# Kernel optimization log

Hardware: AMD Instinct MI355X
Metric: run time of the kernel (lower is better)

The kernel has to match this reference:

```python
import jax, jax.numpy as jnp
import numpy as np

B, T, D = 8, 1024, 1024
SEM = D // 2          # sem_dim_size
STR = D - SEM         # str_dim_size
HALF = SEM // 2       # per-direction semantic slice


def setup_inputs() -> dict:
    key = jax.random.key(0)
    ks = jax.random.split(key, 8)
    s = lambda d: 1.0 / np.sqrt(d)
    return {
        "input": jax.random.normal(ks[0], (B, T, D), jnp.float32),
        "Wtp": jax.random.normal(ks[1], (STR, STR), jnp.float32) * s(STR),
        "btp": jnp.zeros((STR,), jnp.float32),
        "Wtc": jax.random.normal(ks[2], (STR, STR), jnp.float32) * s(STR),
        "btc": jnp.zeros((STR,), jnp.float32),
        "wfi": jax.random.normal(ks[3], (STR,), jnp.float32) * s(STR),
        "Wbil": jax.random.normal(ks[4], (STR, STR), jnp.float32) * s(STR),
        "exparam": jax.random.normal(ks[5], (1, 1, SEM), jnp.float32) * s(SEM),
        "Wfz": jax.random.normal(ks[6], (SEM, 3 * SEM), jnp.float32) * s(3 * SEM),
        "bfz": jnp.zeros((SEM,), jnp.float32),
    }


def reference(input, Wtp, btp, Wtc, btc, wfi, Wbil, exparam, Wfz, bfz):
    b, t, d = input.shape
    dt = input.dtype
    # bidirectional split: interleaved fwd/bwd halves -> semantic / structural views
    x = input.reshape(b, t, 2, d // 2)
    sem_v = jnp.concatenate([x[:, :, 0, :HALF], x[:, :, 1, :HALF]], axis=2)  # (B,T,SEM)
    str_v = jnp.concatenate([x[:, :, 0, HALF:], x[:, :, 1, HALF:]], axis=2)  # (B,T,STR)

    tp = jnp.tanh(str_v @ Wtp.T + btp)
    tc = jnp.tanh(str_v @ Wtc.T + btc)
    # bilinear matrix attention: tp W tc^T -> (B,T,T)
    f_ij = jnp.tanh(jnp.einsum('btd,de,bse->bts', tp, Wbil, tc))
    f_i = jnp.exp(jnp.tanh(str_v @ wfi))  # root scores (B,T)

    eye = jnp.eye(t, dtype=dt)
    A = jnp.exp(f_ij) * (1.0 - eye)             # zero diagonal
    col_sum = jnp.sum(A, axis=1)                # (B,T) in-degree sums
    L = -A + col_sum[:, :, None] * eye          # graph Laplacian
    L_bar = L.at[:, 0, :].set(f_i)              # replace first row with root scores
    LLinv = jnp.linalg.inv(L_bar)               # (B,T,T)

    d0 = f_i * LLinv[:, :, 0]                   # root marginals (B,T)
    diag = jnp.diagonal(LLinv, axis1=-2, axis2=-1)  # (B,T)
    tmp1 = A * diag[:, None, :]                 # A_ij * LLinv_jj
    tmp2 = A * jnp.swapaxes(LLinv, 1, 2)        # A_ij * LLinv_ji
    mask1 = jnp.concatenate([jnp.zeros((b, t, 1), dt), jnp.ones((b, t, t - 1), dt)], axis=2)
    mask2 = jnp.concatenate([jnp.zeros((b, 1, t), dt), jnp.ones((b, t - 1, t), dt)], axis=1)
    dx = mask1 * tmp1 - mask2 * tmp2            # edge marginals (B,T,T)

    d_full = jnp.concatenate([d0[:, None, :], dx], axis=1)   # (B,T+1,T)
    df = jnp.swapaxes(d_full, 1, 2)                          # (B,T,T+1)
    ssr = jnp.concatenate([jnp.broadcast_to(exparam, (b, 1, SEM)), sem_v], axis=1)
    pinp = jnp.einsum('btk,bkd->btd', df, ssr)   # parent-weighted features
    cinp = jnp.einsum('bts,bsd->btd', dx, sem_v) # child-weighted features
    finp = jnp.concatenate([sem_v, pinp, cinp], axis=2)      # (B,T,3*SEM)
    out = jax.nn.relu(finp @ Wfz.T + bfz)
    return (out, df)
```

## Files before the change

kernel.cpp:

```cpp
#include <hip/hip_runtime.h>
#include <math.h>

#define TT 1024
#define NB 64

typedef float f32x4 __attribute__((ext_vector_type(4)));
typedef __bf16 bf16x8 __attribute__((ext_vector_type(8)));

__device__ __forceinline__ float4 ld4(const float* p){ return *(const float4*)p; }
__device__ __forceinline__ float rdlane(float v, int lane){
  return __int_as_float(__builtin_amdgcn_readlane(__float_as_int(v), lane));
}
__device__ __forceinline__ unsigned short bf16rne(float x){
  unsigned u = __float_as_uint(x);
  return (unsigned short)((u + 0x7FFF + ((u >> 16) & 1)) >> 16);
}

template<int EPI, int OUTBF>
__global__ __launch_bounds__(256)
void mgemm_k(const unsigned short* __restrict__ A, const unsigned short* __restrict__ B,
             void* __restrict__ Cv, int K, int lda, int ldb, int ldc,
             long sA, long sB, long sC,
             const float* __restrict__ bias,
             const float* __restrict__ e1, long sE1, const float* __restrict__ e2)
{
  const int bz = blockIdx.z;
  A += (long)bz * sA; B += (long)bz * sB;
  __shared__ char lds[12288];
  char* As = lds;
  char* Bs = lds + 4096;
  const int tid = threadIdx.x;
  const int l = tid & 63, wid = tid >> 6;
  const int wr = wid >> 1, wc = wid & 1;
  const int m0 = blockIdx.y * 64, n0 = blockIdx.x * 128;
  const int lrow = l & 15, lslot = (l >> 4) << 4;
  f32x4 acc[2][4] = {};

  for (int kk = 0; kk < K; kk += 32) {
    {
      int row = tid >> 2, c16 = (tid & 3) << 4;
      int sw = c16 ^ (((row >> 1) & 3) << 4);
      uint4 va = *(const uint4*)(A + (long)(m0 + row) * lda + kk + (c16 >> 1));
      *(uint4*)(As + row * 64 + sw) = va;
    }
#pragma unroll
    for (int i = 0; i < 2; ++i) {
      int idx = i * 256 + tid;
      int row = idx >> 2, c16 = (idx & 3) << 4;
      int sw = c16 ^ (((row >> 1) & 3) << 4);
      uint4 vb = *(const uint4*)(B + (long)(n0 + row) * ldb + kk + (c16 >> 1));
      *(uint4*)(Bs + row * 64 + sw) = vb;
    }
    __syncthreads();
    bf16x8 af[2], bfr[4];
#pragma unroll
    for (int t = 0; t < 2; ++t) {
      int ra = wr * 32 + t * 16 + lrow;
      af[t]  = *(const bf16x8*)(As + ra * 64 + (lslot ^ (((ra >> 1) & 3) << 4)));
    }
#pragma unroll
    for (int t = 0; t < 4; ++t) {
      int rb = wc * 64 + t * 16 + lrow;
      bfr[t] = *(const bf16x8*)(Bs + rb * 64 + (lslot ^ (((rb >> 1) & 3) << 4)));
    }
#pragma unroll
    for (int mi = 0; mi < 2; ++mi)
#pragma unroll
      for (int ni = 0; ni < 4; ++ni)
        acc[mi][ni] = __builtin_amdgcn_mfma_f32_16x16x32_bf16(af[mi], bfr[ni], acc[mi][ni], 0, 0, 0);
    __syncthreads();
  }

  float* Cf = (float*)Cv; unsigned short* Cb = (unsigned short*)Cv;
  if (OUTBF) Cb += (long)bz * sC; else Cf += (long)bz * sC;
  if (e1) e1 += (long)bz * sE1;
#pragma unroll
  for (int mi = 0; mi < 2; ++mi)
#pragma unroll
  for (int ni = 0; ni < 4; ++ni)
#pragma unroll
  for (int r = 0; r < 4; ++r) {
    int m = m0 + wr * 32 + mi * 16 + ((l >> 4) << 2) + r;
    int n = n0 + wc * 64 + ni * 16 + (l & 15);
    float v = acc[mi][ni][r];
    if (EPI == 1) v = tanhf(v + bias[n]);
    else if (EPI == 2) v = (m == n) ? 0.f : expf(tanhf(v));
    else if (EPI == 3) v = fmaxf(v + bias[n], 0.f);
    else if (EPI == 4) v = v + e1[m] * e2[n];
    if (OUTBF) Cb[(long)m * ldc + n] = bf16rne(v);
    else       Cf[(long)m * ldc + n] = v;
  }
}

__global__ __launch_bounds__(256)
void mgemm_pc_k(const unsigned short* __restrict__ A1, const unsigned short* __restrict__ A2,
                const unsigned short* __restrict__ B,
                unsigned short* __restrict__ C1, unsigned short* __restrict__ C2,
                int K, int lda, int ldb, int ldc, long sA, long sB, long sC,
                const float* __restrict__ e1, long sE1, const float* __restrict__ e2)
{
  const int z = blockIdx.z;
  const int bz = z & 7;
  const bool second = (z >= 8);
  const unsigned short* A = (second ? A2 : A1) + (long)bz * sA;
  const unsigned short* Bp = B + (long)bz * sB;
  unsigned short* C = (second ? C2 : C1) + (long)bz * sC;
  const float* e1p = second ? nullptr : (e1 + (long)bz * sE1);
  __shared__ char lds[12288];
  char* As = lds; char* Bs = lds + 4096;
  const int tid = threadIdx.x;
  const int l = tid & 63, wid = tid >> 6;
  const int wr = wid >> 1, wc = wid & 1;
  const int m0 = blockIdx.y * 64, n0 = blockIdx.x * 128;
  const int lrow = l & 15, lslot = (l >> 4) << 4;
  f32x4 acc[2][4] = {};
  for (int kk = 0; kk < K; kk += 32) {
    {
      int row = tid >> 2, c16 = (tid & 3) << 4;
      int sw = c16 ^ (((row >> 1) & 3) << 4);
      uint4 va = *(const uint4*)(A + (long)(m0 + row) * lda + kk + (c16 >> 1));
      *(uint4*)(As + row * 64 + sw) = va;
    }
#pragma unroll
    for (int i = 0; i < 2; ++i) {
      int idx = i * 256 + tid;
      int row = idx >> 2, c16 = (idx & 3) << 4;
      int sw = c16 ^ (((row >> 1) & 3) << 4);
      uint4 vb = *(const uint4*)(Bp + (long)(n0 + row) * ldb + kk + (c16 >> 1));
      *(uint4*)(Bs + row * 64 + sw) = vb;
    }
    __syncthreads();
    bf16x8 af[2], bfr[4];
#pragma unroll
    for (int t = 0; t < 2; ++t) {
      int ra = wr * 32 + t * 16 + lrow;
      af[t]  = *(const bf16x8*)(As + ra * 64 + (lslot ^ (((ra >> 1) & 3) << 4)));
    }
#pragma unroll
    for (int t = 0; t < 4; ++t) {
      int rb = wc * 64 + t * 16 + lrow;
      bfr[t] = *(const bf16x8*)(Bs + rb * 64 + (lslot ^ (((rb >> 1) & 3) << 4)));
    }
#pragma unroll
    for (int mi = 0; mi < 2; ++mi)
#pragma unroll
      for (int ni = 0; ni < 4; ++ni)
        acc[mi][ni] = __builtin_amdgcn_mfma_f32_16x16x32_bf16(af[mi], bfr[ni], acc[mi][ni], 0, 0, 0);
    __syncthreads();
  }
#pragma unroll
  for (int mi = 0; mi < 2; ++mi)
#pragma unroll
  for (int ni = 0; ni < 4; ++ni)
#pragma unroll
  for (int r = 0; r < 4; ++r) {
    int m = m0 + wr * 32 + mi * 16 + ((l >> 4) << 2) + r;
    int n = n0 + wc * 64 + ni * 16 + (l & 15);
    float v = acc[mi][ni][r];
    if (e1p) v = v + e1p[m] * e2[n];
    C[(long)m * ldc + n] = bf16rne(v);
  }
}

__global__ void split_k(const float* __restrict__ in, float* __restrict__ sem,
                        float* __restrict__ str, unsigned short* __restrict__ strb){
  long row = blockIdx.x;
  int c = threadIdx.x << 2;
  float4 v = ld4(in + row * 1024 + c);
  bool isStr = (c >= 256 && c < 512) || (c >= 768);
  int off;
  float* dst;
  if (c < 256)      { dst = sem + row * 512 + c;               off = c; }
  else if (c < 512) { dst = str + row * 512 + (c - 256);       off = c - 256; }
  else if (c < 768) { dst = sem + row * 512 + 256 + (c - 512); off = 0; }
  else              { dst = str + row * 512 + 256 + (c - 768); off = 256 + (c - 768); }
  *(float4*)dst = v;
  if (isStr) {
    unsigned lo = bf16rne(v.x) | ((unsigned)bf16rne(v.y) << 16);
    unsigned hi = bf16rne(v.z) | ((unsigned)bf16rne(v.w) << 16);
    uint2 w; w.x = lo; w.y = hi;
    *(uint2*)(strb + row * 512 + off) = w;
  }
}

__global__ void castw3_k(const float* __restrict__ Wtp, const float* __restrict__ Wtc,
                         const float* __restrict__ Wfz,
                         unsigned short* __restrict__ wtpb, unsigned short* __restrict__ wtcb,
                         unsigned short* __restrict__ wfzb){
  long i = ((long)blockIdx.x * 256 + threadIdx.x) << 2;
  const float* src; unsigned short* dst; long off;
  if (i < 262144)      { src = Wtp; dst = wtpb; off = i; }
  else if (i < 524288) { src = Wtc; dst = wtcb; off = i - 262144; }
  else                 { src = Wfz; dst = wfzb; off = i - 524288; }
  float4 v = ld4(src + off);
  unsigned lo = bf16rne(v.x) | ((unsigned)bf16rne(v.y) << 16);
  unsigned hi = bf16rne(v.z) | ((unsigned)bf16rne(v.w) << 16);
  uint2 w; w.x = lo; w.y = hi;
  *(uint2*)(dst + off) = w;
}

__global__ __launch_bounds__(256) void castT_k(const float* __restrict__ src, unsigned short* __restrict__ dst,
                                               int R, int C, long sS, long sD){
  int b = blockIdx.z;
  src += (long)b * sS; dst += (long)b * sD;
  __shared__ float t[32][33];
  int r0 = blockIdx.y * 32, c0 = blockIdx.x * 32;
  int tx = threadIdx.x & 31, ty = threadIdx.x >> 5;
#pragma unroll
  for (int j = 0; j < 32; j += 8)
    t[ty + j][tx] = src[(long)(r0 + ty + j) * C + c0 + tx];
  __syncthreads();
#pragma unroll
  for (int j = 0; j < 32; j += 8)
    dst[(long)(c0 + ty + j) * R + r0 + tx] = bf16rne(t[tx][ty + j]);
}

__global__ void semcopy_k(const float* __restrict__ sem, unsigned short* __restrict__ finpb){
  long idx = ((long)blockIdx.x * 256 + threadIdx.x) << 2;
  long row = idx >> 9; int col = (int)(idx & 511);
  float4 v = ld4(sem + idx);
  unsigned lo = bf16rne(v.x) | ((unsigned)bf16rne(v.y) << 16);
  unsigned hi = bf16rne(v.z) | ((unsigned)bf16rne(v.w) << 16);
  uint2 w; w.x = lo; w.y = hi;
  *(uint2*)(finpb + row * 1536 + col) = w;
}

__global__ void fi_k(const float* __restrict__ str, const float* __restrict__ wfi, float* __restrict__ fi){
  int row = blockIdx.x * 4 + (threadIdx.x >> 6);
  int lane = threadIdx.x & 63;
  const float* p = str + (long)row * 512;
  float acc = 0.f;
  for (int c = lane; c < 512; c += 64) acc = fmaf(p[c], wfi[c], acc);
  for (int off = 32; off; off >>= 1) acc += __shfl_down(acc, off, 64);
  if (lane == 0) fi[row] = expf(tanhf(acc));
}

__global__ void colsum_k(const float* __restrict__ A, float* __restrict__ csp){
  int b = blockIdx.y, rc = blockIdx.z;
  int j = blockIdx.x * 256 + threadIdx.x;
  const float* p = A + (long)b * TT * TT + (long)rc * 128 * TT + j;
  float acc = 0.f;
  for (int i = 0; i < 128; ++i) acc += p[(long)i * TT];
  csp[rc * 8192 + b * TT + j] = acc;
}

__global__ void buildw_k(const float* __restrict__ A, const float* __restrict__ fi,
                         const float* __restrict__ csp, float* __restrict__ W,
                         unsigned short* __restrict__ Ch0, unsigned short* __restrict__ Cl0){
  long idx = (long)blockIdx.x * 256 + threadIdx.x;
  long b = idx >> 20;
  long r = idx & 1048575;
  int i = (int)(r >> 10), j = (int)(r & 1023);
  float v;
  if (i == 0)      v = fi[b * TT + j];
  else if (i == j) {
    v = 0.f;
#pragma unroll
    for (int c = 0; c < 8; ++c) v += csp[c * 8192 + b * TT + j];
  }
  else             v = -A[idx];
  W[idx] = v;
  if (j < 64) {
    unsigned short h = bf16rne(v);
    float hf = __uint_as_float((unsigned)h << 16);
    Ch0[b * 65536 + i * 64 + j] = h;
    Cl0[b * 65536 + i * 64 + j] = bf16rne(v - hf);
  }
}

#define G16C(c) { float bc = rdlane(e[(c)], K16_);               \
                  float z  = piv ? 0.f : e[(c)];                 \
                  e[(c)] = fmaf(-t, bc, z); }
#define G16S(k) { enum { K16_ = (k) };                           \
    float pk = rdlane(e[K16_], K16_);                            \
    float pr = 1.f / pk;                                         \
    float f  = e[K16_];                                          \
    bool piv = (mm == K16_);                                     \
    float t  = piv ? -pr : f * pr;                               \
    G16C(0) G16C(1) G16C(2) G16C(3) G16C(4) G16C(5) G16C(6) G16C(7) \
    G16C(8) G16C(9) G16C(10) G16C(11) G16C(12) G16C(13) G16C(14) G16C(15) \
    e[K16_] = -t; }

__global__ __launch_bounds__(256) void gj_fprep2_k(const float* __restrict__ W,
                                                   float* __restrict__ Rnew,
                                                   unsigned short* __restrict__ RTh, unsigned short* __restrict__ RTl,
                                                   int k0){
  __shared__ float P[64][65];
  __shared__ float Rt[16][68];
  __shared__ float S[64][68];
  int b = blockIdx.x;
  int J = blockIdx.y * 64;
  int tid = threadIdx.x;
  int l = tid & 63, w = tid >> 6;
  int q16 = w << 4;
  int mm = l & 15;
  const float* Wr = W + (long)b * 1048576 + (long)k0 * 1024 + J;
  for (int i = tid; i < 1024; i += 256) {
    int q = i >> 4, j4 = (i & 15) << 2;
    *(float4*)&S[q][j4] = ld4(Wr + (long)q * 1024 + j4);
  }
  const float* Wd = W + (long)b * 1048576 + (long)(k0 + l) * 1024 + k0 + q16;
#pragma unroll
  for (int c = 0; c < 16; c += 4) {
    float4 v = ld4(Wd + c);
    P[l][q16 + c] = v.x; P[l][q16 + c + 1] = v.y;
    P[l][q16 + c + 2] = v.z; P[l][q16 + c + 3] = v.w;
  }
  __syncthreads();
  for (int kb = 0; kb < 4; ++kb) {
    int kbase = kb << 4;
    float e[16];
#pragma unroll
    for (int c = 0; c < 16; ++c) e[c] = P[kbase + mm][kbase + c];
    G16S(0) G16S(1) G16S(2) G16S(3) G16S(4) G16S(5) G16S(6) G16S(7)
    G16S(8) G16S(9) G16S(10) G16S(11) G16S(12) G16S(13) G16S(14) G16S(15)
    float Cc[16];
#pragma unroll
    for (int c = 0; c < 16; ++c) Cc[c] = P[l][kbase + c];
    int c4 = q16 + ((l >> 4) << 2);
    float r0, r1, r2, r3;
    if (w == kb) {
      int g = l >> 4;
      if (g == 0)      { r0 = e[0];  r1 = e[1];  r2 = e[2];  r3 = e[3];  }
      else if (g == 1) { r0 = e[4];  r1 = e[5];  r2 = e[6];  r3 = e[7];  }
      else if (g == 2) { r0 = e[8];  r1 = e[9];  r2 = e[10]; r3 = e[11]; }
      else             { r0 = e[12]; r1 = e[13]; r2 = e[14]; r3 = e[15]; }
    } else {
      r0 = r1 = r2 = r3 = 0.f;
#pragma unroll
      for (int j = 0; j < 16; ++j) {
        float ej = e[j];
        r0 = fmaf(ej, P[kbase + j][c4 + 0], r0);
        r1 = fmaf(ej, P[kbase + j][c4 + 1], r1);
        r2 = fmaf(ej, P[kbase + j][c4 + 2], r2);
        r3 = fmaf(ej, P[kbase + j][c4 + 3], r3);
      }
    }
    Rt[mm][c4 + 0] = r0; Rt[mm][c4 + 1] = r1;
    Rt[mm][c4 + 2] = r2; Rt[mm][c4 + 3] = r3;
    __syncthreads();
    if (l >= kbase && l < kbase + 16) {
#pragma unroll
      for (int c = 0; c < 16; c += 4) {
        float4 v = *(float4*)&Rt[l - kbase][q16 + c];
        P[l][q16 + c] = v.x; P[l][q16 + c + 1] = v.y;
        P[l][q16 + c + 2] = v.z; P[l][q16 + c + 3] = v.w;
      }
    } else {
      float acc[16];
      bool colKb = (w == kb);
#pragma unroll
      for (int c = 0; c < 16; ++c) acc[c] = colKb ? 0.f : P[l][q16 + c];
#pragma unroll
      for (int j = 0; j < 16; ++j) {
        float cj = Cc[j];
        float4 v0 = *(float4*)&Rt[j][q16 + 0];
        float4 v1 = *(float4*)&Rt[j][q16 + 4];
        float4 v2 = *(float4*)&Rt[j][q16 + 8];
        float4 v3 = *(float4*)&Rt[j][q16 + 12];
        acc[0]  = fmaf(-cj, v0.x, acc[0]);  acc[1]  = fmaf(-cj, v0.y, acc[1]);
        acc[2]  = fmaf(-cj, v0.z, acc[2]);  acc[3]  = fmaf(-cj, v0.w, acc[3]);
        acc[4]  = fmaf(-cj, v1.x, acc[4]);  acc[5]  = fmaf(-cj, v1.y, acc[5]);
        acc[6]  = fmaf(-cj, v1.z, acc[6]);  acc[7]  = fmaf(-cj, v1.w, acc[7]);
        acc[8]  = fmaf(-cj, v2.x, acc[8]);  acc[9]  = fmaf(-cj, v2.y, acc[9]);
        acc[10] = fmaf(-cj, v2.z, acc[10]); acc[11] = fmaf(-cj, v2.w, acc[11]);
        acc[12] = fmaf(-cj, v3.x, acc[12]); acc[13] = fmaf(-cj, v3.y, acc[13]);
        acc[14] = fmaf(-cj, v3.z, acc[14]); acc[15] = fmaf(-cj, v3.w, acc[15]);
      }
#pragma unroll
      for (int c = 0; c < 16; ++c) P[l][q16 + c] = acc[c];
    }
    __syncthreads();
  }
  int p = tid & 63;
  float acc2[16] = {};
  for (int q = 0; q < 64; ++q) {
    float d = P[p][q];
#pragma unroll
    for (int c = 0; c < 16; ++c) acc2[c] = fmaf(d, S[q][q16 + c], acc2[c]);
  }
  __syncthreads();
#pragma unroll
  for (int c = 0; c < 16; ++c) {
    int jg = J + q16 + c;
    float v = acc2[c];
    if (jg >= k0 && jg < k0 + 64) v = P[p][jg - k0];
    S[p][q16 + c] = v;
  }
  __syncthreads();
  float* Rb = Rnew + (long)b * 65536 + J;
  for (int i = tid; i < 1024; i += 256) {
    int rr = i >> 4, j4 = (i & 15) << 2;
    *(float4*)(Rb + (long)rr * 1024 + j4) = *(float4*)&S[rr][j4];
  }
  unsigned short* th = RTh + (long)b * 65536 + (long)J * 64;
  unsigned short* tl = RTl + (long)b * 65536 + (long)J * 64;
  for (int i = tid; i < 4096; i += 256) {
    int jl = i >> 6, pp = i & 63;
    float v = S[pp][jl];
    unsigned short h = bf16rne(v);
    float hf = __uint_as_float((unsigned)h << 16);
    th[i] = h;
    tl[i] = bf16rne(v - hf);
  }
}

__global__ __launch_bounds__(256) void gupd_k(const unsigned short* __restrict__ Ch, const unsigned short* __restrict__ Cl,
                                              const unsigned short* __restrict__ RTh, const unsigned short* __restrict__ RTl,
                                              const float* __restrict__ Rnew, float* __restrict__ W,
                                              unsigned short* __restrict__ ChN, unsigned short* __restrict__ ClN, int k0){
  int b = blockIdx.x;
  const unsigned short* Ahp = Ch + (long)b * 65536;
  const unsigned short* Alp = Cl + (long)b * 65536;
  const unsigned short* Bhp = RTh + (long)b * 65536;
  const unsigned short* Blp = RTl + (long)b * 65536;
  const float* Rb = Rnew + (long)b * 65536;
  float* Wb = W + (long)b * 1048576;
  unsigned short* CnH = ChN + (long)b * 65536;
  unsigned short* CnL = ClN + (long)b * 65536;
  const int tid = threadIdx.x, l = tid & 63, wid = tid >> 6;
  const int wr = wid >> 1, wc = wid & 1;
  const int m0 = blockIdx.y * 64, n0 = blockIdx.z * 64;
  const int lrow = l & 15, kc8 = (l >> 4) << 3;
  f32x4 acc[2][2] = {};
#pragma unroll
  for (int kk = 0; kk < 2; ++kk) {
    bf16x8 ah[2], al4[2], bh[2], bl4[2];
#pragma unroll
    for (int t = 0; t < 2; ++t) {
      int ra = m0 + wr * 32 + t * 16 + lrow;
      long offa = (long)ra * 64 + kk * 32 + kc8;
      ah[t]  = *(const bf16x8*)(Ahp + offa);
      al4[t] = *(const bf16x8*)(Alp + offa);
      int rb = n0 + wc * 32 + t * 16 + lrow;
      long offb = (long)rb * 64 + kk * 32 + kc8;
      bh[t]  = *(const bf16x8*)(Bhp + offb);
      bl4[t] = *(const bf16x8*)(Blp + offb);
    }
#pragma unroll
    for (int mi = 0; mi < 2; ++mi)
#pragma unroll
      for (int ni = 0; ni < 2; ++ni) {
        acc[mi][ni] = __builtin_amdgcn_mfma_f32_16x16x32_bf16(ah[mi],  bh[ni],  acc[mi][ni], 0, 0, 0);
        acc[mi][ni] = __builtin_amdgcn_mfma_f32_16x16x32_bf16(ah[mi],  bl4[ni], acc[mi][ni], 0, 0, 0);
        acc[mi][ni] = __builtin_amdgcn_mfma_f32_16x16x32_bf16(al4[mi], bh[ni],  acc[mi][ni], 0, 0, 0);
      }
  }
#pragma unroll
  for (int mi = 0; mi < 2; ++mi)
#pragma unroll
  for (int ni = 0; ni < 2; ++ni)
#pragma unroll
  for (int r = 0; r < 4; ++r) {
    int m = m0 + wr * 32 + mi * 16 + ((l >> 4) << 2) + r;
    int n = n0 + wc * 32 + ni * 16 + (l & 15);
    bool rowK = (m >= k0 && m < k0 + 64);
    bool colK = (n >= k0 && n < k0 + 64);
    float v;
    if (rowK)      v = Rb[(long)(m - k0) * 1024 + n];
    else if (colK) v = -acc[mi][ni][r];
    else           v = Wb[(long)m * 1024 + n] - acc[mi][ni][r];
    Wb[(long)m * 1024 + n] = v;
    int cn = n - k0 - 64;
    if (cn >= 0 && cn < 64) {
      unsigned short h = bf16rne(v);
      float hf = __uint_as_float((unsigned)h << 16);
      CnH[(long)m * 64 + cn] = h;
      CnL[(long)m * 64 + cn] = bf16rne(v - hf);
    }
  }
}

__global__ void ddiag_k(const float* __restrict__ W, const float* __restrict__ fi,
                        float* __restrict__ d0, float* __restrict__ diag, float* __restrict__ dfout){
  int t = blockIdx.x * 256 + threadIdx.x;
  int b = t >> 10, i = t & 1023;
  const float* Wb = W + (long)b * TT * TT;
  float dv = fi[t] * Wb[(long)i * TT];
  d0[t] = dv;
  diag[t] = Wb[(long)i * TT + i];
  dfout[(long)b * TT * 1025 + (long)i * 1025] = dv;
}

__global__ __launch_bounds__(256) void dx_k(const float* __restrict__ A, const float* __restrict__ W,
                                            const float* __restrict__ diag, float* __restrict__ dfout,
                                            unsigned short* __restrict__ dxb, unsigned short* __restrict__ dxTb){
  int b = blockIdx.z;
  int i0 = blockIdx.y * 64, j0 = blockIdx.x * 64;
  const float* Wb = W + (long)b * TT * TT;
  const float* Ab = A + (long)b * TT * TT;
  __shared__ float Ls[64][65];
  __shared__ float Sx[64][65];
  int tid = threadIdx.x;
  for (int idx = tid; idx < 4096; idx += 256) {
    int r = idx >> 6, c = idx & 63;
    Ls[r][c] = Wb[(long)(j0 + r) * TT + i0 + c];
  }
  __syncthreads();
  for (int idx = tid; idx < 4096; idx += 256) {
    int r = idx >> 6, c = idx & 63;
    int i = i0 + r, j = j0 + c;
    float a = Ab[(long)i * TT + j];
    float v = 0.f;
    if (j > 0) v = a * diag[b * TT + j];
    if (i > 0) v -= a * Ls[c][r];
    dxb[(long)b * 1048576 + (long)i * 1024 + j] = bf16rne(v);
    Sx[r][c] = v;
  }
  __syncthreads();
  float* dfb = dfout + (long)b * TT * 1025;
  unsigned short* dtb = dxTb + (long)b * 1048576;
  for (int idx = tid; idx < 4096; idx += 256) {
    int r = idx >> 6, c = idx & 63;
    float v = Sx[c][r];
    dfb[(long)(j0 + r) * 1025 + i0 + 1 + c] = v;
    dtb[(long)(j0 + r) * 1024 + i0 + c] = bf16rne(v);
  }
}

extern "C" void kernel_launch(void* const* d_in, const int* in_sizes, int n_in,
                              void* d_out, int out_size, void* d_ws, size_t ws_size,
                              hipStream_t stream){
  const float* input   = (const float*)d_in[0];
  const float* Wtp     = (const float*)d_in[1];
  const float* btp     = (const float*)d_in[2];
  const float* Wtc     = (const float*)d_in[3];
  const float* btc     = (const float*)d_in[4];
  const float* wfi     = (const float*)d_in[5];
  const float* Wbil    = (const float*)d_in[6];
  const float* exparam = (const float*)d_in[7];
  const float* Wfz     = (const float*)d_in[8];
  const float* bfz     = (const float*)d_in[9];

  if (ws_size < 150000000UL) return;

  float* ws   = (float*)d_ws;
  float* sem   = ws;
  float* strv  = ws + 4194304;
  float* Abuf  = ws + 8388608;
  float* Wbuf  = ws + 16777216;
  unsigned short* strb = (unsigned short*)(ws + 25165824);
  unsigned short* tpb  = (unsigned short*)(ws + 27262976);
  unsigned short* tcb  = (unsigned short*)(ws + 29360128);
  unsigned short* tpwb = (unsigned short*)(ws + 31457280);
  unsigned short* wtpb = (unsigned short*)(ws + 33554432);
  unsigned short* wtcb = (unsigned short*)(ws + 33685504);
  unsigned short* wbilT= (unsigned short*)(ws + 33816576);
  unsigned short* wfzb = (unsigned short*)(ws + 33947648);
  float* fi    = ws + 34340864;
  float* csp   = ws + 34349056;
  float* d0    = ws + 34414592;
  float* dg    = ws + 34422784;
  float* Rnew  = ws + 34463744;
  unsigned short* ChA = (unsigned short*)(ws + 34988032);
  unsigned short* ClA = (unsigned short*)(ws + 35250176);
  unsigned short* ChB = (unsigned short*)(ws + 35512320);
  unsigned short* ClB = (unsigned short*)(ws + 35774464);
  unsigned short* RTh = (unsigned short*)(ws + 36036608);
  unsigned short* RTl = (unsigned short*)(ws + 36298752);
  unsigned short* dxb   = (unsigned short*)strv;
  unsigned short* dxTb  = (unsigned short*)(ws + 25165824);
  unsigned short* semTb = (unsigned short*)(ws + 29360128);
  unsigned short* finpb = (unsigned short*)Abuf;

  float* outp = (float*)d_out;
  float* dfp  = outp + 4194304;

  split_k<<<8192, 256, 0, stream>>>(input, sem, strv, strb);
  castw3_k<<<1280, 256, 0, stream>>>(Wtp, Wtc, Wfz, wtpb, wtcb, wfzb);
  castT_k<<<dim3(16,16,1), 256, 0, stream>>>(Wbil, wbilT, 512, 512, 0, 0);
  fi_k<<<2048, 256, 0, stream>>>(strv, wfi, fi);
  mgemm_k<1,1><<<dim3(4,128,1),256,0,stream>>>(strb, wtpb, tpb, 512, 512, 512, 512, 0,0,0, btp, nullptr,0,nullptr);
  mgemm_k<1,1><<<dim3(4,128,1),256,0,stream>>>(strb, wtcb, tcb, 512, 512, 512, 512, 0,0,0, btc, nullptr,0,nullptr);
  mgemm_k<0,1><<<dim3(4,128,1),256,0,stream>>>(tpb, wbilT, tpwb, 512, 512, 512, 512, 0,0,0, nullptr, nullptr,0,nullptr);
  mgemm_k<2,0><<<dim3(8,16,8),256,0,stream>>>(tpwb, tcb, Abuf, 512, 512, 512, 1024, 524288,524288,1048576, nullptr, nullptr,0,nullptr);
  castT_k<<<dim3(16,32,8), 256, 0, stream>>>(sem, semTb, 1024, 512, 524288, 524288);
  colsum_k<<<dim3(4,8,8),256,0,stream>>>(Abuf, csp);
  buildw_k<<<32768,256,0,stream>>>(Abuf, fi, csp, Wbuf, ChA, ClA);
  for (int s = 0; s < 16; ++s) {
    int k0 = s * NB;
    unsigned short* ChI = (s & 1) ? ChB : ChA;
    unsigned short* ClI = (s & 1) ? ClB : ClA;
    unsigned short* ChO = (s & 1) ? ChA : ChB;
    unsigned short* ClO = (s & 1) ? ClA : ClB;
    gj_fprep2_k<<<dim3(8,16),256,0,stream>>>(Wbuf, Rnew, RTh, RTl, k0);
    gupd_k<<<dim3(8,16,16),256,0,stream>>>(ChI, ClI, RTh, RTl, Rnew, Wbuf, ChO, ClO, k0);
  }
  ddiag_k<<<32,256,0,stream>>>(Wbuf, fi, d0, dg, dfp);
  dx_k<<<dim3(16,16,8),256,0,stream>>>(Abuf, Wbuf, dg, dfp, dxb, dxTb);
  semcopy_k<<<4096,256,0,stream>>>(sem, finpb);
  mgemm_pc_k<<<dim3(4,16,16),256,0,stream>>>(dxTb, dxb, semTb, finpb + 512, finpb + 1024,
                                             1024, 1024, 1024, 1536, 1048576, 524288, 1572864,
                                             d0, 1024, exparam);
  mgemm_k<3,0><<<dim3(4,128,1),256,0,stream>>>(finpb, wfzb, outp, 1536, 1536, 1536, 512, 0,0,0, bfz, nullptr,0,nullptr);
}
```

Measured before the change: 1.038 ms.

## Double Gauss-Jordan panel width to halve inversion launch rounds

Raises the blocked Gauss-Jordan panel size from 64 to 128, so the in-place inversion takes 8 rounds instead of 16 (half the launches and global passes over W). The panel factorization kernel is rewritten for a 128x128 pivot block with a reorganized thread mapping, and the update GEMM uses K=128. Workspace buffers are moved to reuse freed regions. In exchange the panel kernel needs much more shared memory, does more serial work per block with only 128 blocks, and the update GEMM does twice the inner-product work per round.

```diff
diff --git a/kernel.cpp b/kernel.cpp
--- a/kernel.cpp
+++ b/kernel.cpp
@@ -2,7 +2,7 @@
 #include <math.h>
 
 #define TT 1024
-#define NB 64
+#define NB 128
 
 typedef float f32x4 __attribute__((ext_vector_type(4)));
 typedef __bf16 bf16x8 __attribute__((ext_vector_type(8)));
@@ -260,11 +260,11 @@
   }
   else             v = -A[idx];
   W[idx] = v;
-  if (j < 64) {
+  if (j < 128) {
     unsigned short h = bf16rne(v);
     float hf = __uint_as_float((unsigned)h << 16);
-    Ch0[b * 65536 + i * 64 + j] = h;
-    Cl0[b * 65536 + i * 64 + j] = bf16rne(v - hf);
+    Ch0[b * 131072 + i * 128 + j] = h;
+    Cl0[b * 131072 + i * 128 + j] = bf16rne(v - hf);
   }
 }
 
@@ -281,33 +281,34 @@
     G16C(8) G16C(9) G16C(10) G16C(11) G16C(12) G16C(13) G16C(14) G16C(15) \
     e[K16_] = -t; }
 
-__global__ __launch_bounds__(256) void gj_fprep2_k(const float* __restrict__ W,
+__global__ __launch_bounds__(256) void gj_fprep3_k(const float* __restrict__ W,
                                                    float* __restrict__ Rnew,
                                                    unsigned short* __restrict__ RTh, unsigned short* __restrict__ RTl,
                                                    int k0){
-  __shared__ float P[64][65];
-  __shared__ float Rt[16][68];
-  __shared__ float S[64][68];
+  __shared__ float P[128][129];
+  __shared__ float Rt[16][132];
+  __shared__ float S[128][68];
   int b = blockIdx.x;
   int J = blockIdx.y * 64;
   int tid = threadIdx.x;
-  int l = tid & 63, w = tid >> 6;
-  int q16 = w << 4;
+  int l = tid & 63;
+  int r2 = tid & 127, hh = tid >> 7;
   int mm = l & 15;
+  int g = tid >> 4;
   const float* Wr = W + (long)b * 1048576 + (long)k0 * 1024 + J;
-  for (int i = tid; i < 1024; i += 256) {
+  for (int i = tid; i < 2048; i += 256) {
     int q = i >> 4, j4 = (i & 15) << 2;
     *(float4*)&S[q][j4] = ld4(Wr + (long)q * 1024 + j4);
   }
-  const float* Wd = W + (long)b * 1048576 + (long)(k0 + l) * 1024 + k0 + q16;
-#pragma unroll
-  for (int c = 0; c < 16; c += 4) {
+  const float* Wd = W + (long)b * 1048576 + (long)(k0 + r2) * 1024 + k0 + hh * 64;
+#pragma unroll
+  for (int c = 0; c < 64; c += 4) {
     float4 v = ld4(Wd + c);
-    P[l][q16 + c] = v.x; P[l][q16 + c + 1] = v.y;
-    P[l][q16 + c + 2] = v.z; P[l][q16 + c + 3] = v.w;
+    P[r2][hh * 64 + c]     = v.x; P[r2][hh * 64 + c + 1] = v.y;
+    P[r2][hh * 64 + c + 2] = v.z; P[r2][hh * 64 + c + 3] = v.w;
   }
   __syncthreads();
-  for (int kb = 0; kb < 4; ++kb) {
+  for (int kb = 0; kb < 8; ++kb) {
     int kbase = kb << 4;
     float e[16];
 #pragma unroll
@@ -316,87 +317,95 @@
     G16S(8) G16S(9) G16S(10) G16S(11) G16S(12) G16S(13) G16S(14) G16S(15)
     float Cc[16];
 #pragma unroll
-    for (int c = 0; c < 16; ++c) Cc[c] = P[l][kbase + c];
-    int c4 = q16 + ((l >> 4) << 2);
-    float r0, r1, r2, r3;
-    if (w == kb) {
-      int g = l >> 4;
-      if (g == 0)      { r0 = e[0];  r1 = e[1];  r2 = e[2];  r3 = e[3];  }
-      else if (g == 1) { r0 = e[4];  r1 = e[5];  r2 = e[6];  r3 = e[7];  }
-      else if (g == 2) { r0 = e[8];  r1 = e[9];  r2 = e[10]; r3 = e[11]; }
-      else             { r0 = e[12]; r1 = e[13]; r2 = e[14]; r3 = e[15]; }
-    } else {
-      r0 = r1 = r2 = r3 = 0.f;
-#pragma unroll
-      for (int j = 0; j < 16; ++j) {
-        float ej = e[j];
-        r0 = fmaf(ej, P[kbase + j][c4 + 0], r0);
-        r1 = fmaf(ej, P[kbase + j][c4 + 1], r1);
-        r2 = fmaf(ej, P[kbase + j][c4 + 2], r2);
-        r3 = fmaf(ej, P[kbase + j][c4 + 3], r3);
+    for (int c = 0; c < 16; ++c) Cc[c] = P[r2][kbase + c];
+    {
+      int col0 = g << 3;
+      float rr[8];
+      if (g == (kb << 1)) {
+#pragma unroll
+        for (int cc = 0; cc < 8; ++cc) rr[cc] = e[cc];
+      } else if (g == (kb << 1) + 1) {
+#pragma unroll
+        for (int cc = 0; cc < 8; ++cc) rr[cc] = e[8 + cc];
+      } else {
+#pragma unroll
+        for (int cc = 0; cc < 8; ++cc) rr[cc] = 0.f;
+#pragma unroll
+        for (int j = 0; j < 16; ++j) {
+          float ej = e[j];
+#pragma unroll
+          for (int cc = 0; cc < 8; ++cc)
+            rr[cc] = fmaf(ej, P[kbase + j][col0 + cc], rr[cc]);
+        }
       }
-    }
-    Rt[mm][c4 + 0] = r0; Rt[mm][c4 + 1] = r1;
-    Rt[mm][c4 + 2] = r2; Rt[mm][c4 + 3] = r3;
+#pragma unroll
+      for (int cc = 0; cc < 8; ++cc) Rt[mm][col0 + cc] = rr[cc];
+    }
     __syncthreads();
-    if (l >= kbase && l < kbase + 16) {
-#pragma unroll
-      for (int c = 0; c < 16; c += 4) {
-        float4 v = *(float4*)&Rt[l - kbase][q16 + c];
-        P[l][q16 + c] = v.x; P[l][q16 + c + 1] = v.y;
-        P[l][q16 + c + 2] = v.z; P[l][q16 + c + 3] = v.w;
+    if (r2 >= kbase && r2 < kbase + 16) {
+#pragma unroll
+      for (int c = 0; c < 64; c += 4) {
+        float4 v = *(float4*)&Rt[r2 - kbase][hh * 64 + c];
+        P[r2][hh * 64 + c]     = v.x; P[r2][hh * 64 + c + 1] = v.y;
+        P[r2][hh * 64 + c + 2] = v.z; P[r2][hh * 64 + c + 3] = v.w;
       }
     } else {
-      float acc[16];
-      bool colKb = (w == kb);
-#pragma unroll
-      for (int c = 0; c < 16; ++c) acc[c] = colKb ? 0.f : P[l][q16 + c];
-#pragma unroll
-      for (int j = 0; j < 16; ++j) {
-        float cj = Cc[j];
-        float4 v0 = *(float4*)&Rt[j][q16 + 0];
-        float4 v1 = *(float4*)&Rt[j][q16 + 4];
-        float4 v2 = *(float4*)&Rt[j][q16 + 8];
-        float4 v3 = *(float4*)&Rt[j][q16 + 12];
-        acc[0]  = fmaf(-cj, v0.x, acc[0]);  acc[1]  = fmaf(-cj, v0.y, acc[1]);
-        acc[2]  = fmaf(-cj, v0.z, acc[2]);  acc[3]  = fmaf(-cj, v0.w, acc[3]);
-        acc[4]  = fmaf(-cj, v1.x, acc[4]);  acc[5]  = fmaf(-cj, v1.y, acc[5]);
-        acc[6]  = fmaf(-cj, v1.z, acc[6]);  acc[7]  = fmaf(-cj, v1.w, acc[7]);
-        acc[8]  = fmaf(-cj, v2.x, acc[8]);  acc[9]  = fmaf(-cj, v2.y, acc[9]);
-        acc[10] = fmaf(-cj, v2.z, acc[10]); acc[11] = fmaf(-cj, v2.w, acc[11]);
-        acc[12] = fmaf(-cj, v3.x, acc[12]); acc[13] = fmaf(-cj, v3.y, acc[13]);
-        acc[14] = fmaf(-cj, v3.z, acc[14]); acc[15] = fmaf(-cj, v3.w, acc[15]);
+#pragma unroll
+      for (int cb = 0; cb < 4; ++cb) {
+        int cbase = hh * 64 + (cb << 4);
+        float acc[16];
+#pragma unroll
+        for (int c = 0; c < 16; ++c) {
+          int cg = cbase + c;
+          bool inK = (cg >= kbase && cg < kbase + 16);
+          acc[c] = inK ? 0.f : P[r2][cg];
+        }
+#pragma unroll
+        for (int j = 0; j < 16; ++j) {
+          float cj = Cc[j];
+          float4 v0 = *(float4*)&Rt[j][cbase + 0];
+          float4 v1 = *(float4*)&Rt[j][cbase + 4];
+          float4 v2 = *(float4*)&Rt[j][cbase + 8];
+          float4 v3 = *(float4*)&Rt[j][cbase + 12];
+          acc[0]  = fmaf(-cj, v0.x, acc[0]);  acc[1]  = fmaf(-cj, v0.y, acc[1]);
+          acc[2]  = fmaf(-cj, v0.z, acc[2]);  acc[3]  = fmaf(-cj, v0.w, acc[3]);
+          acc[4]  = fmaf(-cj, v1.x, acc[4]);  acc[5]  = fmaf(-cj, v1.y, acc[5]);
+          acc[6]  = fmaf(-cj, v1.z, acc[6]);  acc[7]  = fmaf(-cj, v1.w, acc[7]);
+          acc[8]  = fmaf(-cj, v2.x, acc[8]);  acc[9]  = fmaf(-cj, v2.y, acc[9]);
+          acc[10] = fmaf(-cj, v2.z, acc[10]); acc[11] = fmaf(-cj, v2.w, acc[11]);
+          acc[12] = fmaf(-cj, v3.x, acc[12]); acc[13] = fmaf(-cj, v3.y, acc[13]);
+          acc[14] = fmaf(-cj, v3.z, acc[14]); acc[15] = fmaf(-cj, v3.w, acc[15]);
+        }
+#pragma unroll
+        for (int c = 0; c < 16; ++c) P[r2][cbase + c] = acc[c];
       }
-#pragma unroll
-      for (int c = 0; c < 16; ++c) P[l][q16 + c] = acc[c];
     }
     __syncthreads();
   }
-  int p = tid & 63;
-  float acc2[16] = {};
-  for (int q = 0; q < 64; ++q) {
-    float d = P[p][q];
-#pragma unroll
-    for (int c = 0; c < 16; ++c) acc2[c] = fmaf(d, S[q][q16 + c], acc2[c]);
+  float a2[32] = {};
+  for (int q = 0; q < 128; ++q) {
+    float d = P[r2][q];
+#pragma unroll
+    for (int c = 0; c < 32; ++c) a2[c] = fmaf(d, S[q][hh * 32 + c], a2[c]);
   }
   __syncthreads();
 #pragma unroll
-  for (int c = 0; c < 16; ++c) {
-    int jg = J + q16 + c;
-    float v = acc2[c];
-    if (jg >= k0 && jg < k0 + 64) v = P[p][jg - k0];
-    S[p][q16 + c] = v;
+  for (int c = 0; c < 32; ++c) {
+    int jg = J + hh * 32 + c;
+    float v = a2[c];
+    if (jg >= k0 && jg < k0 + 128) v = P[r2][jg - k0];
+    S[r2][hh * 32 + c] = v;
   }
   __syncthreads();
-  float* Rb = Rnew + (long)b * 65536 + J;
-  for (int i = tid; i < 1024; i += 256) {
-    int rr = i >> 4, j4 = (i & 15) << 2;
-    *(float4*)(Rb + (long)rr * 1024 + j4) = *(float4*)&S[rr][j4];
-  }
-  unsigned short* th = RTh + (long)b * 65536 + (long)J * 64;
-  unsigned short* tl = RTl + (long)b * 65536 + (long)J * 64;
-  for (int i = tid; i < 4096; i += 256) {
-    int jl = i >> 6, pp = i & 63;
+  float* Rb = Rnew + (long)b * 131072 + J;
+  for (int i = tid; i < 2048; i += 256) {
+    int rr2 = i >> 4, j4 = (i & 15) << 2;
+    *(float4*)(Rb + (long)rr2 * 1024 + j4) = *(float4*)&S[rr2][j4];
+  }
+  unsigned short* th = RTh + (long)b * 131072 + (long)J * 128;
+  unsigned short* tl = RTl + (long)b * 131072 + (long)J * 128;
+  for (int i = tid; i < 8192; i += 256) {
+    int jl = i >> 7, pp = i & 127;
     float v = S[pp][jl];
     unsigned short h = bf16rne(v);
     float hf = __uint_as_float((unsigned)h << 16);
@@ -410,30 +419,30 @@
                                               const float* __restrict__ Rnew, float* __restrict__ W,
                                               unsigned short* __restrict__ ChN, unsigned short* __restrict__ ClN, int k0){
   int b = blockIdx.x;
-  const unsigned short* Ahp = Ch + (long)b * 65536;
-  const unsigned short* Alp = Cl + (long)b * 65536;
-  const unsigned short* Bhp = RTh + (long)b * 65536;
-  const unsigned short* Blp = RTl + (long)b * 65536;
-  const float* Rb = Rnew + (long)b * 65536;
+  const unsigned short* Ahp = Ch + (long)b * 131072;
+  const unsigned short* Alp = Cl + (long)b * 131072;
+  const unsigned short* Bhp = RTh + (long)b * 131072;
+  const unsigned short* Blp = RTl + (long)b * 131072;
+  const float* Rb = Rnew + (long)b * 131072;
   float* Wb = W + (long)b * 1048576;
-  unsigned short* CnH = ChN + (long)b * 65536;
-  unsigned short* CnL = ClN + (long)b * 65536;
+  unsigned short* CnH = ChN + (long)b * 131072;
+  unsigned short* CnL = ClN + (long)b * 131072;
   const int tid = threadIdx.x, l = tid & 63, wid = tid >> 6;
   const int wr = wid >> 1, wc = wid & 1;
   const int m0 = blockIdx.y * 64, n0 = blockIdx.z * 64;
   const int lrow = l & 15, kc8 = (l >> 4) << 3;
   f32x4 acc[2][2] = {};
 #pragma unroll
-  for (int kk = 0; kk < 2; ++kk) {
+  for (int kk = 0; kk < 4; ++kk) {
     bf16x8 ah[2], al4[2], bh[2], bl4[2];
 #pragma unroll
     for (int t = 0; t < 2; ++t) {
       int ra = m0 + wr * 32 + t * 16 + lrow;
-      long offa = (long)ra * 64 + kk * 32 + kc8;
+      long offa = (long)ra * 128 + kk * 32 + kc8;
       ah[t]  = *(const bf16x8*)(Ahp + offa);
       al4[t] = *(const bf16x8*)(Alp + offa);
       int rb = n0 + wc * 32 + t * 16 + lrow;
-      long offb = (long)rb * 64 + kk * 32 + kc8;
+      long offb = (long)rb * 128 + kk * 32 + kc8;
       bh[t]  = *(const bf16x8*)(Bhp + offb);
       bl4[t] = *(const bf16x8*)(Blp + offb);
     }
@@ -454,19 +463,19 @@
   for (int r = 0; r < 4; ++r) {
     int m = m0 + wr * 32 + mi * 16 + ((l >> 4) << 2) + r;
     int n = n0 + wc * 32 + ni * 16 + (l & 15);
-    bool rowK = (m >= k0 && m < k0 + 64);
-    bool colK = (n >= k0 && n < k0 + 64);
+    bool rowK = (m >= k0 && m < k0 + NB);
+    bool colK = (n >= k0 && n < k0 + NB);
     float v;
     if (rowK)      v = Rb[(long)(m - k0) * 1024 + n];
     else if (colK) v = -acc[mi][ni][r];
     else           v = Wb[(long)m * 1024 + n] - acc[mi][ni][r];
     Wb[(long)m * 1024 + n] = v;
-    int cn = n - k0 - 64;
-    if (cn >= 0 && cn < 64) {
+    int cn = n - k0 - NB;
+    if (cn >= 0 && cn < NB) {
       unsigned short h = bf16rne(v);
       float hf = __uint_as_float((unsigned)h << 16);
-      CnH[(long)m * 64 + cn] = h;
-      CnL[(long)m * 64 + cn] = bf16rne(v - hf);
+      CnH[(long)m * 128 + cn] = h;
+      CnL[(long)m * 128 + cn] = bf16rne(v - hf);
     }
   }
 }
@@ -551,13 +560,13 @@
   float* csp   = ws + 34349056;
   float* d0    = ws + 34414592;
   float* dg    = ws + 34422784;
-  float* Rnew  = ws + 34463744;
-  unsigned short* ChA = (unsigned short*)(ws + 34988032);
-  unsigned short* ClA = (unsigned short*)(ws + 35250176);
-  unsigned short* ChB = (unsigned short*)(ws + 35512320);
-  unsigned short* ClB = (unsigned short*)(ws + 35774464);
-  unsigned short* RTh = (unsigned short*)(ws + 36036608);
-  unsigned short* RTl = (unsigned short*)(ws + 36298752);
+  float* Rnew  = ws + 34430976;
+  unsigned short* ChA = (unsigned short*)(ws + 25165824);
+  unsigned short* ClA = (unsigned short*)(ws + 25690112);
+  unsigned short* ChB = (unsigned short*)(ws + 26214400);
+  unsigned short* ClB = (unsigned short*)(ws + 26738688);
+  unsigned short* RTh = (unsigned short*)(ws + 31457280);
+  unsigned short* RTl = (unsigned short*)(ws + 31981568);
   unsigned short* dxb   = (unsigned short*)strv;
   unsigned short* dxTb  = (unsigned short*)(ws + 25165824);
   unsigned short* semTb = (unsigned short*)(ws + 29360128);
@@ -577,13 +586,13 @@
   castT_k<<<dim3(16,32,8), 256, 0, stream>>>(sem, semTb, 1024, 512, 524288, 524288);
   colsum_k<<<dim3(4,8,8),256,0,stream>>>(Abuf, csp);
   buildw_k<<<32768,256,0,stream>>>(Abuf, fi, csp, Wbuf, ChA, ClA);
-  for (int s = 0; s < 16; ++s) {
+  for (int s = 0; s < 8; ++s) {
     int k0 = s * NB;
     unsigned short* ChI = (s & 1) ? ChB : ChA;
     unsigned short* ClI = (s & 1) ? ClB : ClA;
     unsigned short* ChO = (s & 1) ? ChA : ChB;
     unsigned short* ClO = (s & 1) ? ClA : ClB;
-    gj_fprep2_k<<<dim3(8,16),256,0,stream>>>(Wbuf, Rnew, RTh, RTl, k0);
+    gj_fprep3_k<<<dim3(8,16),256,0,stream>>>(Wbuf, Rnew, RTh, RTl, k0);
     gupd_k<<<dim3(8,16,16),256,0,stream>>>(ChI, ClI, RTh, RTl, Rnew, Wbuf, ChO, ClO, k0);
   }
   ddiag_k<<<32,256,0,stream>>>(Wbuf, fi, d0, dg, dfp);
```

Result: slower. 1.197 ms (+15.3%).

## Fuse score GEMM epilogue with column sums and Laplacian construction

Applied to the files above, without the earlier changes.

The bilinear score GEMM now writes both the exp(tanh) attention matrix and its negation into the Laplacian buffer, and computes per-tile column partial sums through wave shuffles and LDS. This removes the separate column-sum kernel and the full 32 MB reread/rewrite pass that built the Laplacian. A small fixup kernel then sets the root row and diagonal from the partial sums and fills the first panel of the bf16 hi/lo buffers. The GEMM epilogue now issues twice the stores, and the workspace offsets are shifted to make room for the 16 partial column-sum slices.

```diff
diff --git a/kernel.cpp b/kernel.cpp
--- a/kernel.cpp
+++ b/kernel.cpp
@@ -84,12 +84,89 @@
     int n = n0 + wc * 64 + ni * 16 + (l & 15);
     float v = acc[mi][ni][r];
     if (EPI == 1) v = tanhf(v + bias[n]);
-    else if (EPI == 2) v = (m == n) ? 0.f : expf(tanhf(v));
     else if (EPI == 3) v = fmaxf(v + bias[n], 0.f);
     else if (EPI == 4) v = v + e1[m] * e2[n];
     if (OUTBF) Cb[(long)m * ldc + n] = bf16rne(v);
     else       Cf[(long)m * ldc + n] = v;
   }
+}
+
+__global__ __launch_bounds__(256)
+void mgemm_score_k(const unsigned short* __restrict__ A, const unsigned short* __restrict__ B,
+                   float* __restrict__ Ab, float* __restrict__ Wb, float* __restrict__ csp)
+{
+  const int bz = blockIdx.z;
+  A += (long)bz * 524288; B += (long)bz * 524288;
+  __shared__ char lds[12288];
+  __shared__ float csb[2][128];
+  char* As = lds; char* Bs = lds + 4096;
+  const int tid = threadIdx.x;
+  const int l = tid & 63, wid = tid >> 6;
+  const int wr = wid >> 1, wc = wid & 1;
+  const int m0 = blockIdx.y * 64, n0 = blockIdx.x * 128;
+  const int lrow = l & 15, lslot = (l >> 4) << 4;
+  f32x4 acc[2][4] = {};
+  for (int kk = 0; kk < 512; kk += 32) {
+    {
+      int row = tid >> 2, c16 = (tid & 3) << 4;
+      int sw = c16 ^ (((row >> 1) & 3) << 4);
+      uint4 va = *(const uint4*)(A + (long)(m0 + row) * 512 + kk + (c16 >> 1));
+      *(uint4*)(As + row * 64 + sw) = va;
+    }
+#pragma unroll
+    for (int i = 0; i < 2; ++i) {
+      int idx = i * 256 + tid;
+      int row = idx >> 2, c16 = (idx & 3) << 4;
+      int sw = c16 ^ (((row >> 1) & 3) << 4);
+      uint4 vb = *(const uint4*)(B + (long)(n0 + row) * 512 + kk + (c16 >> 1));
+      *(uint4*)(Bs + row * 64 + sw) = vb;
+    }
+    __syncthreads();
+    bf16x8 af[2], bfr[4];
+#pragma unroll
+    for (int t = 0; t < 2; ++t) {
+      int ra = wr * 32 + t * 16 + lrow;
+      af[t]  = *(const bf16x8*)(As + ra * 64 + (lslot ^ (((ra >> 1) & 3) << 4)));
+    }
+#pragma unroll
+    for (int t = 0; t < 4; ++t) {
+      int rb = wc * 64 + t * 16 + lrow;
+      bfr[t] = *(const bf16x8*)(Bs + rb * 64 + (lslot ^ (((rb >> 1) & 3) << 4)));
+    }
+#pragma unroll
+    for (int mi = 0; mi < 2; ++mi)
+#pragma unroll
+      for (int ni = 0; ni < 4; ++ni)
+        acc[mi][ni] = __builtin_amdgcn_mfma_f32_16x16x32_bf16(af[mi], bfr[ni], acc[mi][ni], 0, 0, 0);
+    __syncthreads();
+  }
+  Ab += (long)bz * 1048576; Wb += (long)bz * 1048576;
+  float cst[4] = {0.f, 0.f, 0.f, 0.f};
+#pragma unroll
+  for (int mi = 0; mi < 2; ++mi)
+#pragma unroll
+  for (int ni = 0; ni < 4; ++ni)
+#pragma unroll
+  for (int r = 0; r < 4; ++r) {
+    int m = m0 + wr * 32 + mi * 16 + ((l >> 4) << 2) + r;
+    int n = n0 + wc * 64 + ni * 16 + (l & 15);
+    float v = (m == n) ? 0.f : expf(tanhf(acc[mi][ni][r]));
+    Ab[(long)m * 1024 + n] = v;
+    Wb[(long)m * 1024 + n] = -v;
+    cst[ni] += v;
+  }
+#pragma unroll
+  for (int ni = 0; ni < 4; ++ni) {
+    cst[ni] += __shfl_xor(cst[ni], 16, 64);
+    cst[ni] += __shfl_xor(cst[ni], 32, 64);
+  }
+  if ((l >> 4) == 0) {
+#pragma unroll
+    for (int ni = 0; ni < 4; ++ni) csb[wr][wc * 64 + ni * 16 + (l & 15)] = cst[ni];
+  }
+  __syncthreads();
+  if (tid < 128)
+    csp[(long)blockIdx.y * 8192 + bz * 1024 + n0 + tid] = csb[0][tid] + csb[1][tid];
 }
 
 __global__ __launch_bounds__(256)
@@ -235,36 +312,42 @@
   if (lane == 0) fi[row] = expf(tanhf(acc));
 }
 
-__global__ void colsum_k(const float* __restrict__ A, float* __restrict__ csp){
-  int b = blockIdx.y, rc = blockIdx.z;
-  int j = blockIdx.x * 256 + threadIdx.x;
-  const float* p = A + (long)b * TT * TT + (long)rc * 128 * TT + j;
-  float acc = 0.f;
-  for (int i = 0; i < 128; ++i) acc += p[(long)i * TT];
-  csp[rc * 8192 + b * TT + j] = acc;
-}
-
-__global__ void buildw_k(const float* __restrict__ A, const float* __restrict__ fi,
-                         const float* __restrict__ csp, float* __restrict__ W,
-                         unsigned short* __restrict__ Ch0, unsigned short* __restrict__ Cl0){
-  long idx = (long)blockIdx.x * 256 + threadIdx.x;
-  long b = idx >> 20;
-  long r = idx & 1048575;
-  int i = (int)(r >> 10), j = (int)(r & 1023);
-  float v;
-  if (i == 0)      v = fi[b * TT + j];
-  else if (i == j) {
-    v = 0.f;
-#pragma unroll
-    for (int c = 0; c < 8; ++c) v += csp[c * 8192 + b * TT + j];
-  }
-  else             v = -A[idx];
-  W[idx] = v;
-  if (j < 64) {
+__global__ void buildfix_k(const float* __restrict__ csp, const float* __restrict__ fi,
+                           float* __restrict__ W,
+                           unsigned short* __restrict__ Ch0, unsigned short* __restrict__ Cl0){
+  int rc = blockIdx.x, b = blockIdx.y;
+  int tid = threadIdx.x;
+  __shared__ float cs[64];
+  int i0 = rc * 64;
+  if (tid < 64) {
+    float s = 0.f;
+#pragma unroll
+    for (int p = 0; p < 16; ++p) s += csp[(long)p * 8192 + b * 1024 + i0 + tid];
+    cs[tid] = s;
+  }
+  __syncthreads();
+  float* Wb = W + (long)b * 1048576;
+  const float* fib = fi + b * 1024;
+  if (rc == 0) {
+    for (int j = tid; j < 1024; j += 256) Wb[j] = fib[j];
+  }
+  if (tid < 64) {
+    int i = i0 + tid;
+    if (i != 0) Wb[(long)i * 1024 + i] = cs[tid];
+  }
+  unsigned short* ChB_ = Ch0 + b * 65536;
+  unsigned short* ClB_ = Cl0 + b * 65536;
+  for (int e = tid; e < 4096; e += 256) {
+    int ii = e >> 6, j = e & 63;
+    int i = i0 + ii;
+    float v;
+    if (i == 0)      v = fib[j];
+    else if (i == j) v = cs[ii];
+    else             v = Wb[(long)i * 1024 + j];
     unsigned short h = bf16rne(v);
     float hf = __uint_as_float((unsigned)h << 16);
-    Ch0[b * 65536 + i * 64 + j] = h;
-    Cl0[b * 65536 + i * 64 + j] = bf16rne(v - hf);
+    ChB_[(long)i * 64 + j] = h;
+    ClB_[(long)i * 64 + j] = bf16rne(v - hf);
   }
 }
 
@@ -532,7 +615,7 @@
   const float* Wfz     = (const float*)d_in[8];
   const float* bfz     = (const float*)d_in[9];
 
-  if (ws_size < 150000000UL) return;
+  if (ws_size < 147000000UL) return;
 
   float* ws   = (float*)d_ws;
   float* sem   = ws;
@@ -549,15 +632,15 @@
   unsigned short* wfzb = (unsigned short*)(ws + 33947648);
   float* fi    = ws + 34340864;
   float* csp   = ws + 34349056;
-  float* d0    = ws + 34414592;
-  float* dg    = ws + 34422784;
-  float* Rnew  = ws + 34463744;
-  unsigned short* ChA = (unsigned short*)(ws + 34988032);
-  unsigned short* ClA = (unsigned short*)(ws + 35250176);
-  unsigned short* ChB = (unsigned short*)(ws + 35512320);
-  unsigned short* ClB = (unsigned short*)(ws + 35774464);
-  unsigned short* RTh = (unsigned short*)(ws + 36036608);
-  unsigned short* RTl = (unsigned short*)(ws + 36298752);
+  float* d0    = ws + 34480128;
+  float* dg    = ws + 34488320;
+  float* Rnew  = ws + 34496512;
+  unsigned short* ChA = (unsigned short*)(ws + 35020800);
+  unsigned short* ClA = (unsigned short*)(ws + 35282944);
+  unsigned short* ChB = (unsigned short*)(ws + 35545088);
+  unsigned short* ClB = (unsigned short*)(ws + 35807232);
+  unsigned short* RTh = (unsigned short*)(ws + 36069376);
+  unsigned short* RTl = (unsigned short*)(ws + 36331520);
   unsigned short* dxb   = (unsigned short*)strv;
   unsigned short* dxTb  = (unsigned short*)(ws + 25165824);
   unsigned short* semTb = (unsigned short*)(ws + 29360128);
@@ -573,10 +656,9 @@
   mgemm_k<1,1><<<dim3(4,128,1),256,0,stream>>>(strb, wtpb, tpb, 512, 512, 512, 512, 0,0,0, btp, nullptr,0,nullptr);
   mgemm_k<1,1><<<dim3(4,128,1),256,0,stream>>>(strb, wtcb, tcb, 512, 512, 512, 512, 0,0,0, btc, nullptr,0,nullptr);
   mgemm_k<0,1><<<dim3(4,128,1),256,0,stream>>>(tpb, wbilT, tpwb, 512, 512, 512, 512, 0,0,0, nullptr, nullptr,0,nullptr);
-  mgemm_k<2,0><<<dim3(8,16,8),256,0,stream>>>(tpwb, tcb, Abuf, 512, 512, 512, 1024, 524288,524288,1048576, nullptr, nullptr,0,nullptr);
+  mgemm_score_k<<<dim3(8,16,8),256,0,stream>>>(tpwb, tcb, Abuf, Wbuf, csp);
   castT_k<<<dim3(16,32,8), 256, 0, stream>>>(sem, semTb, 1024, 512, 524288, 524288);
-  colsum_k<<<dim3(4,8,8),256,0,stream>>>(Abuf, csp);
-  buildw_k<<<32768,256,0,stream>>>(Abuf, fi, csp, Wbuf, ChA, ClA);
+  buildfix_k<<<dim3(16,8),256,0,stream>>>(csp, fi, Wbuf, ChA, ClA);
   for (int s = 0; s < 16; ++s) {
     int k0 = s * NB;
     unsigned short* ChI = (s & 1) ? ChB : ChA;
```

Result: no change. 1.024 ms (-1.3%).
